# Kernel tuning notes

Measured on AMD Instinct MI355X. Metric: run time of the kernel, lower is better.

## Reference

```python
import jax, jax.numpy as jnp
import numpy as np

DIM = 1024
H_HEADS = 16


def setup_inputs() -> dict:
    key = jax.random.key(0)
    ks = jax.random.split(key, 12)
    h, w = 48, 80
    hw = h * w
    n_frames, n_sel = 11, 384
    wscale = 1.0 / np.sqrt(DIM).astype(np.float32)
    return {
        "feats_cur": jax.random.normal(ks[0], (1, DIM, h, w), jnp.float32),
        "ps": jax.random.normal(ks[1], (1, DIM, h, w), jnp.float32),
        "feats_ref": jax.random.normal(ks[2], (n_frames, DIM, h, w), jnp.float32),
        "ext_mem": jax.random.normal(ks[3], (24000, DIM), jnp.float32),
        "glob_cache": jax.random.normal(ks[4], (4000, DIM), jnp.float32),
        "Wq": jax.random.normal(ks[5], (DIM, DIM), jnp.float32) * wscale,
        "Wk": jax.random.normal(ks[6], (DIM, DIM), jnp.float32) * wscale,
        "Wv": jax.random.normal(ks[7], (DIM, DIM), jnp.float32) * wscale,
        "Wo": jax.random.normal(ks[8], (DIM, DIM), jnp.float32) * wscale,
        "ref_sel_idx": jax.random.randint(ks[9], (n_frames, n_sel), 0, hw, jnp.int32),
        "mem_idx": jax.random.randint(ks[10], (2000,), 0, 24000, jnp.int32),
        "glob_idx": jax.random.randint(ks[11], (2000,), 0, 4000, jnp.int32),
    }


def reference(feats_cur, ps, feats_ref, ext_mem, glob_cache, Wq, Wk, Wv, Wo,
              ref_sel_idx, mem_idx, glob_idx):
    b, dim, h, w = feats_cur.shape
    hw = h * w
    # current-frame pixels with positional encoding -> queries [hw, dim]
    q_in = (feats_cur + ps)[0].reshape(dim, hw).T
    # reference frames + ps -> [F, hw, dim], sparse randperm-style subsample via precomputed indices
    ref = (feats_ref + ps).reshape(-1, dim, hw).transpose(0, 2, 1)
    sel = jnp.take_along_axis(ref, ref_sel_idx[:, :, None], axis=1).reshape(-1, dim)
    # concat with subsampled external memory and global cache pixels
    k_in = jnp.concatenate([sel, ext_mem[mem_idx], glob_cache[glob_idx]], axis=0)  # [Nk, dim]
    dh = dim // H_HEADS
    scale = 1.0 / np.sqrt(dh).astype(np.float32)
    q = (q_in @ Wq).reshape(hw, H_HEADS, dh)
    k = (k_in @ Wk).reshape(-1, H_HEADS, dh)
    v = (k_in @ Wv).reshape(-1, H_HEADS, dh)
    logits = jnp.einsum('qhd,khd->hqk', q, k) * scale  # [H, hw, Nk]
    attn = jax.nn.softmax(logits, axis=-1)
    ctx = jnp.einsum('hqk,khd->qhd', attn, v).reshape(hw, dim)
    out = q_in + ctx @ Wo  # residual, like MEGA relation module
    # back to [1, dim, h, w] as in update_lm_pixel_with_transpose
    return out.T.reshape(1, dim, h, w)
```

## Files before the change

kernel.cpp:

```cpp
#include <hip/hip_runtime.h>

using u16 = unsigned short;
using bf16x8 = __attribute__((ext_vector_type(8))) short;
using f32x4  = __attribute__((ext_vector_type(4))) float;

#define DIM   1024
#define HW    3840
#define NSEL  4224
#define NK    8224
#define NKPAD 8320
#define NH    16
#define KVB   64
#define THR   50.0f

typedef __attribute__((address_space(1))) const unsigned GU;
typedef __attribute__((address_space(3))) unsigned LU;

__device__ __forceinline__ u16 f2bf(float x) {
    unsigned u = __float_as_uint(x);
    return (u16)((u + 0x7FFFu + ((u >> 16) & 1u)) >> 16);
}

__device__ __forceinline__ float exp2fast(float x) {
    return __builtin_amdgcn_exp2f(x);
}

__global__ void prep_kernel(const float* __restrict__ Wq, const float* __restrict__ Wk,
                            const float* __restrict__ Wv, const float* __restrict__ Wo,
                            const float* __restrict__ fc, const float* __restrict__ ps,
                            const float* __restrict__ fr, const float* __restrict__ em,
                            const float* __restrict__ gc, const int* __restrict__ sel,
                            const int* __restrict__ midx, const int* __restrict__ gidx,
                            u16* __restrict__ WT, u16* __restrict__ qin, u16* __restrict__ kin) {
    const int b = blockIdx.x;
    const int tid = threadIdx.x;
    if (b < 4096) {
        const int zz = b >> 10, yy = (b >> 5) & 31, xx = b & 31;
        const float* src = zz == 0 ? Wq : zz == 1 ? Wk : zz == 2 ? Wv : Wo;
        u16* dst = WT + (size_t)zz * DIM * DIM;
        __shared__ float t[32][33];
        const int n0 = xx * 32, k0 = yy * 32;
        const int tx = tid & 31, ty = tid >> 5;
#pragma unroll
        for (int j = 0; j < 4; ++j)
            t[ty + 8 * j][tx] = src[(size_t)(k0 + ty + 8 * j) * DIM + n0 + tx];
        __syncthreads();
#pragma unroll
        for (int j = 0; j < 4; ++j)
            dst[(size_t)(n0 + ty + 8 * j) * DIM + k0 + tx] = f2bf(t[tx][ty + 8 * j]);
    } else if (b < 7936) {
        const int bb = b - 4096;
        const int xx = bb % 120, yy = bb / 120;
        __shared__ float t[32][33];
        const int p0 = xx * 32, d0 = yy * 32;
        const int tx = tid & 31, ty = tid >> 5;
#pragma unroll
        for (int j = 0; j < 4; ++j) {
            int d = d0 + ty + 8 * j;
            t[ty + 8 * j][tx] = fc[(size_t)d * HW + p0 + tx] + ps[(size_t)d * HW + p0 + tx];
        }
        __syncthreads();
#pragma unroll
        for (int j = 0; j < 4; ++j)
            qin[(size_t)(p0 + ty + 8 * j) * DIM + d0 + tx] = f2bf(t[tx][ty + 8 * j]);
    } else {
        const int row = b - 7936;
        u16* dst = kin + (size_t)row * DIM;
        const int t = tid;
        if (row < NSEL) {
            const int f = row / 384;
            const int idx = sel[row];
            const float* base = fr + (size_t)f * DIM * HW + idx;
#pragma unroll
            for (int j = 0; j < 4; ++j) {
                int d = t + 256 * j;
                dst[d] = f2bf(base[(size_t)d * HW] + ps[(size_t)d * HW + idx]);
            }
        } else if (row < NSEL + 2000) {
            const float* src = em + (size_t)midx[row - NSEL] * DIM;
#pragma unroll
            for (int j = 0; j < 4; ++j) { int d = t + 256 * j; dst[d] = f2bf(src[d]); }
        } else if (row < NK) {
            const float* src = gc + (size_t)gidx[row - (NSEL + 2000)] * DIM;
#pragma unroll
            for (int j = 0; j < 4; ++j) { int d = t + 256 * j; dst[d] = f2bf(src[d]); }
        } else {
#pragma unroll
            for (int j = 0; j < 4; ++j) dst[t + 256 * j] = 0;
        }
    }
}

__device__ __forceinline__ void gemm_bt_body(const u16* __restrict__ A,
                                             const u16* __restrict__ B,
                                             void* __restrict__ Cout,
                                             const float* __restrict__ r1,
                                             const float* __restrict__ r2,
                                             int ldc, int mode, float scale,
                                             int bx, int by) {
    __shared__ __align__(16) u16 As[2][128 * 64];
    __shared__ __align__(16) u16 Bs[2][128 * 64];
    const int tid = threadIdx.x;
    const int l = tid & 63;
    const int wv = tid >> 6;
    const int wr = (wv >> 1) * 64, wc = (wv & 1) * 64;
    const int g = l >> 4, lo = l & 15;
    const size_t bm = (size_t)by * 128, bn = (size_t)bx * 128;
    const f32x4 fzero = {0.f, 0.f, 0.f, 0.f};

    f32x4 acc[4][4];
#pragma unroll
    for (int i = 0; i < 4; ++i)
#pragma unroll
        for (int j = 0; j < 4; ++j) acc[i][j] = fzero;

#define GSTAGE(BUF, KT)                                                                         \
    {                                                                                           \
        const int k0_ = (KT) * 64;                                                              \
        _Pragma("unroll") for (int q = 0; q < 4; ++q) {                                         \
            const int idx = q * 256 + tid;                                                      \
            const int row = idx >> 3, c8 = idx & 7;                                             \
            const int scol = (c8 ^ (row & 7)) * 8;                                              \
            const int dbase = q * 2048 + wv * 512;                                              \
            __builtin_amdgcn_global_load_lds((GU*)(A + (bm + row) * DIM + k0_ + scol),          \
                                             (LU*)&As[BUF][dbase], 16, 0, 0);                   \
            __builtin_amdgcn_global_load_lds((GU*)(B + (bn + row) * DIM + k0_ + scol),          \
                                             (LU*)&Bs[BUF][dbase], 16, 0, 0);                   \
        }                                                                                       \
    }

#define GCOMPUTE(BUF)                                                                           \
    {                                                                                           \
        _Pragma("unroll") for (int ks = 0; ks < 2; ++ks) {                                      \
            bf16x8 af[4], bfv[4];                                                               \
            _Pragma("unroll") for (int mi = 0; mi < 4; ++mi) {                                  \
                const int row = wr + mi * 16 + lo;                                              \
                const int sw = (ks * 4 + g) ^ (row & 7);                                        \
                af[mi] = *(const bf16x8*)(&As[BUF][row * 64 + sw * 8]);                         \
            }                                                                                   \
            _Pragma("unroll") for (int ni = 0; ni < 4; ++ni) {                                  \
                const int row = wc + ni * 16 + lo;                                              \
                const int sw = (ks * 4 + g) ^ (row & 7);                                        \
                bfv[ni] = *(const bf16x8*)(&Bs[BUF][row * 64 + sw * 8]);                        \
            }                                                                                   \
            _Pragma("unroll") for (int mi = 0; mi < 4; ++mi)                                    \
                _Pragma("unroll") for (int ni = 0; ni < 4; ++ni)                                \
                    acc[mi][ni] = __builtin_amdgcn_mfma_f32_16x16x32_bf16(af[mi], bfv[ni], acc[mi][ni], 0, 0, 0); \
        }                                                                                       \
    }

    GSTAGE(0, 0)
    asm volatile("s_waitcnt vmcnt(0)" ::: "memory");
    __syncthreads();

#pragma unroll 1
    for (int kt = 0; kt < 16; kt += 2) {
        GSTAGE(1, kt + 1)
        GCOMPUTE(0)
        asm volatile("s_waitcnt vmcnt(0)" ::: "memory");
        __syncthreads();
        if (kt + 2 < 16) GSTAGE(0, kt + 2)
        GCOMPUTE(1)
        asm volatile("s_waitcnt vmcnt(0)" ::: "memory");
        __syncthreads();
    }
#undef GCOMPUTE
#undef GSTAGE

    if (mode == 0) {
        u16* C = (u16*)Cout;
#pragma unroll
        for (int mi = 0; mi < 4; ++mi)
#pragma unroll
            for (int ni = 0; ni < 4; ++ni)
#pragma unroll
                for (int r = 0; r < 4; ++r) {
                    size_t m = bm + wr + mi * 16 + g * 4 + r;
                    size_t n = bn + wc + ni * 16 + lo;
                    C[m * (size_t)ldc + n] = f2bf(acc[mi][ni][r] * scale);
                }
    } else if (mode == 2) {
        u16* C = (u16*)Cout;
#pragma unroll
        for (int mi = 0; mi < 4; ++mi)
#pragma unroll
            for (int ni = 0; ni < 4; ++ni)
#pragma unroll
                for (int r = 0; r < 4; ++r) {
                    size_t m = bm + wr + mi * 16 + g * 4 + r;
                    size_t n = bn + wc + ni * 16 + lo;
                    size_t o = (n >> 6) * ((size_t)NKPAD * 64) + m * 64 + (n & 63);
                    C[o] = f2bf(acc[mi][ni][r] * scale);
                }
    } else {
        float* C = (float*)Cout;
#pragma unroll
        for (int mi = 0; mi < 4; ++mi)
#pragma unroll
            for (int ni = 0; ni < 4; ++ni)
#pragma unroll
                for (int r = 0; r < 4; ++r) {
                    size_t m = bm + wr + mi * 16 + g * 4 + r;
                    size_t n = bn + wc + ni * 16 + lo;
                    size_t o = m * (size_t)ldc + n;
                    C[o] = acc[mi][ni][r] + r1[o] + r2[o];
                }
    }
}

__global__ __launch_bounds__(256, 2) void proj_kernel(const u16* __restrict__ qin,
                                                      const u16* __restrict__ kin,
                                                      const u16* __restrict__ WT,
                                                      u16* __restrict__ Qp,
                                                      u16* __restrict__ Kp,
                                                      u16* __restrict__ Vt) {
    const int b = blockIdx.x;
    if (b < 240) {
        gemm_bt_body(qin, WT, Qp, nullptr, nullptr, 1024, 0, 0.18033688f, b % 8, b / 8);
    } else if (b < 760) {
        const int bb = b - 240;
        gemm_bt_body(kin, WT + 1048576, Kp, nullptr, nullptr, 1024, 2, 1.0f, bb % 8, bb / 8);
    } else {
        const int bb = b - 760;
        gemm_bt_body(WT + 2097152, kin, Vt, nullptr, nullptr, NKPAD, 0, 1.0f, bb % 65, bb / 65);
    }
}

__global__ __launch_bounds__(256, 2) void outproj_kernel(const u16* __restrict__ WTo,
                                                         const u16* __restrict__ ctx,
                                                         float* __restrict__ out,
                                                         const float* __restrict__ fc,
                                                         const float* __restrict__ ps) {
    gemm_bt_body(WTo, ctx, out, fc, ps, HW, 1, 1.0f, blockIdx.x, blockIdx.y);
}

__global__ __launch_bounds__(256, 3) void attn_kernel(const u16* __restrict__ Q,
                                                      const u16* __restrict__ Kh,
                                                      const u16* __restrict__ Vt,
                                                      u16* __restrict__ ctx) {
    __shared__ __align__(16) u16 Kl[2][4096];
    __shared__ __align__(16) u16 Vl[2][4096];
    __shared__ float invl_s[4][32];
    const int h = blockIdx.x;
    const int tid = threadIdx.x;
    const int l = tid & 63, wv = tid >> 6;
    const int g = l >> 4, lo = l & 15;
    const int hoff = h * 64;
    const int qw = blockIdx.y * 128 + wv * 32;
    const f32x4 fzero = {0.f, 0.f, 0.f, 0.f};
    const int sig = (lo >> 2) * 8 + (lo & 3);

    const u16* Ksrc = Kh + (size_t)h * NKPAD * 64;
    const u16* Vsrc = Vt + (size_t)hoff * NKPAD;

    bf16x8 qa[2][2];
#pragma unroll
    for (int mi = 0; mi < 2; ++mi)
#pragma unroll
        for (int ks = 0; ks < 2; ++ks)
            qa[mi][ks] = *(const bf16x8*)(Q + (size_t)(qw + mi * 16 + lo) * DIM + hoff + ks * 32 + g * 8);

    f32x4 acc[2][4];
#pragma unroll
    for (int mi = 0; mi < 2; ++mi)
#pragma unroll
        for (int ni = 0; ni < 4; ++ni) acc[mi][ni] = fzero;
    float mrow[2] = {-1e30f, -1e30f};
    float lsum[2] = {0.f, 0.f};
    float pmax[2] = {-1e30f, -1e30f};

#define STAGE(BUF, IT)                                                                          \
    {                                                                                           \
        const int kks = (IT) * KVB;                                                             \
        _Pragma("unroll") for (int j = 0; j < 2; ++j) {                                         \
            const int inst = wv * 2 + j;                                                        \
            const int r_ = inst * 8 + (l >> 3);                                                 \
            const int c_ = l & 7;                                                               \
            const int hk_ = ((l >> 3) & 3) | ((inst & 1) << 2);                                 \
            const u16* gK = Ksrc + (size_t)(kks + r_) * 64 + ((c_ ^ hk_) * 8);                  \
            __builtin_amdgcn_global_load_lds((GU*)gK, (LU*)&Kl[BUF][inst * 512], 16, 0, 0);     \
            const u16* gV = Vsrc + (size_t)r_ * NKPAD + kks + ((c_ ^ (r_ & 7)) * 8);            \
            __builtin_amdgcn_global_load_lds((GU*)gV, (LU*)&Vl[BUF][inst * 512], 16, 0, 0);     \
        }                                                                                       \
    }

#define COMPUTE(BUF, NT, NS)                                                                    \
    {                                                                                           \
        f32x4 S[2][4];                                                                          \
        _Pragma("unroll") for (int kp = 0; kp < (NT) / 2; ++kp) {                               \
            bf16x8 kf[2][2];                                                                    \
            _Pragma("unroll") for (int k2 = 0; k2 < 2; ++k2)                                    \
                _Pragma("unroll") for (int ks = 0; ks < 2; ++ks) {                              \
                    const int kt = kp * 2 + k2;                                                 \
                    const int row = (kt >> 1) * 32 + (kt & 1) * 4 + sig;                        \
                    const int hk_ = (row & 3) | (((row >> 3) & 1) << 2);                        \
                    const int ck = (ks * 4 + g) ^ hk_;                                          \
                    kf[k2][ks] = *(const bf16x8*)(&Kl[BUF][row * 64 + ck * 8]);                 \
                }                                                                               \
            _Pragma("unroll") for (int mi = 0; mi < 2; ++mi)                                    \
                _Pragma("unroll") for (int k2 = 0; k2 < 2; ++k2) {                              \
                    f32x4 s_ = __builtin_amdgcn_mfma_f32_16x16x32_bf16(kf[k2][0], qa[mi][0], fzero, 0, 0, 0); \
                    S[mi][kp * 2 + k2] = __builtin_amdgcn_mfma_f32_16x16x32_bf16(kf[k2][1], qa[mi][1], s_, 0, 0, 0); \
                }                                                                               \
        }                                                                                       \
        _Pragma("unroll") for (int mi = 0; mi < 2; ++mi)                                        \
            _Pragma("unroll") for (int kt = 0; kt < (NT); ++kt) {                               \
                f32x4 sv = S[mi][kt];                                                           \
                pmax[mi] = fmaxf(pmax[mi], fmaxf(fmaxf(sv[0], sv[1]), fmaxf(sv[2], sv[3])));    \
            }                                                                                   \
        if (__any(fmaxf(pmax[0] - mrow[0], pmax[1] - mrow[1]) > THR)) {                         \
            _Pragma("unroll") for (int mi = 0; mi < 2; ++mi) {                                  \
                float v = pmax[mi];                                                             \
                v = fmaxf(v, __shfl_xor(v, 16));                                                \
                v = fmaxf(v, __shfl_xor(v, 32));                                                \
                float mn = fmaxf(mrow[mi], v);                                                  \
                float fct = exp2fast(mrow[mi] - mn);                                            \
                mrow[mi] = mn;                                                                  \
                lsum[mi] *= fct;                                                                \
                _Pragma("unroll") for (int r = 0; r < 4; ++r) {                                 \
                    float fr_ = __shfl(fct, g * 4 + r);                                         \
                    _Pragma("unroll") for (int ni = 0; ni < 4; ++ni) acc[mi][ni][r] *= fr_;     \
                }                                                                               \
            }                                                                                   \
        }                                                                                       \
        _Pragma("unroll") for (int s = 0; s < (NS); ++s) {                                      \
            bf16x8 vb[4];                                                                       \
            _Pragma("unroll") for (int ni = 0; ni < 4; ++ni) {                                  \
                const int row = ni * 16 + lo;                                                   \
                const int ck = (s * 4 + g) ^ (row & 7);                                         \
                vb[ni] = *(const bf16x8*)(&Vl[BUF][row * 64 + ck * 8]);                         \
            }                                                                                   \
            _Pragma("unroll") for (int mi = 0; mi < 2; ++mi) {                                  \
                float p0 = exp2fast(S[mi][2 * s][0] - mrow[mi]);                                \
                float p1 = exp2fast(S[mi][2 * s][1] - mrow[mi]);                                \
                float p2 = exp2fast(S[mi][2 * s][2] - mrow[mi]);                                \
                float p3 = exp2fast(S[mi][2 * s][3] - mrow[mi]);                                \
                float p4 = exp2fast(S[mi][2 * s + 1][0] - mrow[mi]);                            \
                float p5 = exp2fast(S[mi][2 * s + 1][1] - mrow[mi]);                            \
                float p6 = exp2fast(S[mi][2 * s + 1][2] - mrow[mi]);                            \
                float p7 = exp2fast(S[mi][2 * s + 1][3] - mrow[mi]);                            \
                lsum[mi] += ((p0 + p1) + (p2 + p3)) + ((p4 + p5) + (p6 + p7));                  \
                union { unsigned u[4]; bf16x8 v; } pu;                                          \
                asm("v_cvt_pk_bf16_f32 %0, %1, %2" : "=v"(pu.u[0]) : "v"(p0), "v"(p1));         \
                asm("v_cvt_pk_bf16_f32 %0, %1, %2" : "=v"(pu.u[1]) : "v"(p2), "v"(p3));         \
                asm("v_cvt_pk_bf16_f32 %0, %1, %2" : "=v"(pu.u[2]) : "v"(p4), "v"(p5));         \
                asm("v_cvt_pk_bf16_f32 %0, %1, %2" : "=v"(pu.u[3]) : "v"(p6), "v"(p7));         \
                _Pragma("unroll") for (int ni = 0; ni < 4; ++ni)                                \
                    acc[mi][ni] = __builtin_amdgcn_mfma_f32_16x16x32_bf16(pu.v, vb[ni], acc[mi][ni], 0, 0, 0); \
            }                                                                                   \
        }                                                                                       \
    }

    STAGE(0, 0)
    asm volatile("s_waitcnt vmcnt(0)" ::: "memory");
    __syncthreads();

#pragma unroll 1
    for (int it = 0; it < 128; it += 2) {
        STAGE(1, it + 1)
        COMPUTE(0, 4, 2)
        asm volatile("s_waitcnt vmcnt(0)" ::: "memory");
        __syncthreads();
        STAGE(0, it + 2)
        COMPUTE(1, 4, 2)
        asm volatile("s_waitcnt vmcnt(0)" ::: "memory");
        __syncthreads();
    }
    COMPUTE(0, 2, 1)
#undef COMPUTE
#undef STAGE

#pragma unroll
    for (int mi = 0; mi < 2; ++mi) {
        float t = lsum[mi];
        t += __shfl_xor(t, 16);
        t += __shfl_xor(t, 32);
        lsum[mi] = t;
    }
    if (l < 16) {
        invl_s[wv][lo] = 1.0f / lsum[0];
        invl_s[wv][16 + lo] = 1.0f / lsum[1];
    }
#pragma unroll
    for (int mi = 0; mi < 2; ++mi)
#pragma unroll
        for (int ni = 0; ni < 4; ++ni)
#pragma unroll
            for (int r = 0; r < 4; ++r) {
                float val = acc[mi][ni][r] * invl_s[wv][mi * 16 + g * 4 + r];
                ctx[(size_t)(qw + mi * 16 + g * 4 + r) * DIM + hoff + ni * 16 + lo] = f2bf(val);
            }
}

extern "C" void kernel_launch(void* const* d_in, const int* in_sizes, int n_in,
                              void* d_out, int out_size, void* d_ws, size_t ws_size,
                              hipStream_t stream) {
    const float* fc  = (const float*)d_in[0];
    const float* ps  = (const float*)d_in[1];
    const float* fr  = (const float*)d_in[2];
    const float* em  = (const float*)d_in[3];
    const float* gc  = (const float*)d_in[4];
    const float* Wq  = (const float*)d_in[5];
    const float* Wk  = (const float*)d_in[6];
    const float* Wv  = (const float*)d_in[7];
    const float* Wo  = (const float*)d_in[8];
    const int* sel   = (const int*)d_in[9];
    const int* midx  = (const int*)d_in[10];
    const int* gidx  = (const int*)d_in[11];

    char* w = (char*)d_ws;
    u16* WT  = (u16*)(w);
    u16* qin = (u16*)(w + 8388608ull);
    u16* kin = (u16*)(w + 16252928ull);
    u16* Qp  = (u16*)(w + 33292288ull);
    u16* Kp  = (u16*)(w + 41156608ull);
    u16* Vt  = (u16*)(w + 58195968ull);
    u16* ctx = (u16*)(w + 75235328ull);
    float* out = (float*)d_out;

    prep_kernel<<<dim3(16256), dim3(256), 0, stream>>>(Wq, Wk, Wv, Wo, fc, ps, fr, em, gc,
                                                       sel, midx, gidx, WT, qin, kin);
    proj_kernel<<<dim3(1280), dim3(256), 0, stream>>>(qin, kin, WT, Qp, Kp, Vt);

    attn_kernel<<<dim3(NH, 30), dim3(256), 0, stream>>>(Qp, Kp, Vt, ctx);

    outproj_kernel<<<dim3(30, 8), dim3(256), 0, stream>>>(WT + 3145728, ctx, out, fc, ps);
}
```

Measured before the change: 403.2 us.

## Split attention KV range across wave pairs and merge partial softmax states

The attention kernel now gives each block 64 query rows instead of 128 and splits the key/value sequence between two wave pairs. Each pair streams its own half in 32-key tiles and keeps its own running max and sum. The two partial results are then merged through shared memory using a log-sum-exp rescale. The grid doubles to 960 blocks and the occupancy hint rises to 4 blocks per CU, to improve latency hiding and CU fill. In exchange, the kernel has smaller MFMA tiles per barrier, more synchronisation, and an extra reduction epilogue.

```diff
diff --git a/kernel.cpp b/kernel.cpp
--- a/kernel.cpp
+++ b/kernel.cpp
@@ -10,7 +10,6 @@
 #define NK    8224
 #define NKPAD 8320
 #define NH    16
-#define KVB   64
 #define THR   50.0f
 
 typedef __attribute__((address_space(1))) const unsigned GU;
@@ -234,21 +233,25 @@
     gemm_bt_body(WTo, ctx, out, fc, ps, HW, 1, 1.0f, blockIdx.x, blockIdx.y);
 }
 
-__global__ __launch_bounds__(256, 3) void attn_kernel(const u16* __restrict__ Q,
+__global__ __launch_bounds__(256, 4) void attn_kernel(const u16* __restrict__ Q,
                                                       const u16* __restrict__ Kh,
                                                       const u16* __restrict__ Vt,
                                                       u16* __restrict__ ctx) {
-    __shared__ __align__(16) u16 Kl[2][4096];
-    __shared__ __align__(16) u16 Vl[2][4096];
-    __shared__ float invl_s[4][32];
+    __shared__ __align__(16) u16 Kst[2][2][2048];
+    __shared__ __align__(16) u16 Vst[2][2][2048];
+    __shared__ float mlb[2][2][32][2];
+    __shared__ float mbuf2[2][32][20];
     const int h = blockIdx.x;
     const int tid = threadIdx.x;
     const int l = tid & 63, wv = tid >> 6;
+    const int qh = wv & 1, kh = wv >> 1;
     const int g = l >> 4, lo = l & 15;
     const int hoff = h * 64;
-    const int qw = blockIdx.y * 128 + wv * 32;
+    const int qw = blockIdx.y * 64 + qh * 32;
     const f32x4 fzero = {0.f, 0.f, 0.f, 0.f};
     const int sig = (lo >> 2) * 8 + (lo & 3);
+    const int W0 = kh * 128;
+    const int nw = 128 + kh;
 
     const u16* Ksrc = Kh + (size_t)h * NKPAD * 64;
     const u16* Vsrc = Vt + (size_t)hoff * NKPAD;
@@ -269,45 +272,46 @@
     float lsum[2] = {0.f, 0.f};
     float pmax[2] = {-1e30f, -1e30f};
 
-#define STAGE(BUF, IT)                                                                          \
+#define STAGE32(BUF, IT)                                                                        \
     {                                                                                           \
-        const int kks = (IT) * KVB;                                                             \
-        _Pragma("unroll") for (int j = 0; j < 2; ++j) {                                         \
-            const int inst = wv * 2 + j;                                                        \
-            const int r_ = inst * 8 + (l >> 3);                                                 \
-            const int c_ = l & 7;                                                               \
-            const int hk_ = ((l >> 3) & 3) | ((inst & 1) << 2);                                 \
-            const u16* gK = Ksrc + (size_t)(kks + r_) * 64 + ((c_ ^ hk_) * 8);                  \
-            __builtin_amdgcn_global_load_lds((GU*)gK, (LU*)&Kl[BUF][inst * 512], 16, 0, 0);     \
-            const u16* gV = Vsrc + (size_t)r_ * NKPAD + kks + ((c_ ^ (r_ & 7)) * 8);            \
-            __builtin_amdgcn_global_load_lds((GU*)gV, (LU*)&Vl[BUF][inst * 512], 16, 0, 0);     \
-        }                                                                                       \
-    }
-
-#define COMPUTE(BUF, NT, NS)                                                                    \
+        const int kk_ = (W0 + (IT)) * 32;                                                       \
+        _Pragma("unroll") for (int jj = 0; jj < 2; ++jj) {                                      \
+            const int j = qh * 2 + jj;                                                          \
+            const int rk = j * 8 + (l >> 3);                                                    \
+            const int hkk = (rk & 3) | (((rk >> 3) & 1) << 2);                                  \
+            const u16* gK = Ksrc + (size_t)(kk_ + rk) * 64 + (((l & 7) ^ hkk) * 8);             \
+            __builtin_amdgcn_global_load_lds((GU*)gK, (LU*)&Kst[kh][BUF][j * 512], 16, 0, 0);   \
+            const int xu = (l & 7) ^ (l >> 3);                                                  \
+            const int dv = 2 * rk + (xu >> 2);                                                  \
+            const u16* gV = Vsrc + (size_t)dv * NKPAD + kk_ + ((xu & 3) * 8);                   \
+            __builtin_amdgcn_global_load_lds((GU*)gV, (LU*)&Vst[kh][BUF][j * 512], 16, 0, 0);   \
+        }                                                                                       \
+    }
+
+#define COMPUTE32(BUF)                                                                          \
     {                                                                                           \
-        f32x4 S[2][4];                                                                          \
-        _Pragma("unroll") for (int kp = 0; kp < (NT) / 2; ++kp) {                               \
-            bf16x8 kf[2][2];                                                                    \
-            _Pragma("unroll") for (int k2 = 0; k2 < 2; ++k2)                                    \
-                _Pragma("unroll") for (int ks = 0; ks < 2; ++ks) {                              \
-                    const int kt = kp * 2 + k2;                                                 \
-                    const int row = (kt >> 1) * 32 + (kt & 1) * 4 + sig;                        \
-                    const int hk_ = (row & 3) | (((row >> 3) & 1) << 2);                        \
-                    const int ck = (ks * 4 + g) ^ hk_;                                          \
-                    kf[k2][ks] = *(const bf16x8*)(&Kl[BUF][row * 64 + ck * 8]);                 \
-                }                                                                               \
-            _Pragma("unroll") for (int mi = 0; mi < 2; ++mi)                                    \
-                _Pragma("unroll") for (int k2 = 0; k2 < 2; ++k2) {                              \
-                    f32x4 s_ = __builtin_amdgcn_mfma_f32_16x16x32_bf16(kf[k2][0], qa[mi][0], fzero, 0, 0, 0); \
-                    S[mi][kp * 2 + k2] = __builtin_amdgcn_mfma_f32_16x16x32_bf16(kf[k2][1], qa[mi][1], s_, 0, 0, 0); \
-                }                                                                               \
-        }                                                                                       \
-        _Pragma("unroll") for (int mi = 0; mi < 2; ++mi)                                        \
-            _Pragma("unroll") for (int kt = 0; kt < (NT); ++kt) {                               \
-                f32x4 sv = S[mi][kt];                                                           \
-                pmax[mi] = fmaxf(pmax[mi], fmaxf(fmaxf(sv[0], sv[1]), fmaxf(sv[2], sv[3])));    \
-            }                                                                                   \
+        bf16x8 kf0, kf1, kf2, kf3;                                                              \
+        {                                                                                       \
+            const int r0_ = sig, r1_ = sig + 4;                                                 \
+            const int h0_ = (r0_ & 3) | (((r0_ >> 3) & 1) << 2);                                \
+            const int h1_ = (r1_ & 3) | (((r1_ >> 3) & 1) << 2);                                \
+            kf0 = *(const bf16x8*)(&Kst[kh][BUF][r0_ * 64 + ((0 + g) ^ h0_) * 8]);              \
+            kf1 = *(const bf16x8*)(&Kst[kh][BUF][r0_ * 64 + ((4 + g) ^ h0_) * 8]);              \
+            kf2 = *(const bf16x8*)(&Kst[kh][BUF][r1_ * 64 + ((0 + g) ^ h1_) * 8]);              \
+            kf3 = *(const bf16x8*)(&Kst[kh][BUF][r1_ * 64 + ((4 + g) ^ h1_) * 8]);              \
+        }                                                                                       \
+        f32x4 S0[2], S1[2];                                                                     \
+        _Pragma("unroll") for (int mi = 0; mi < 2; ++mi) {                                      \
+            f32x4 s_ = __builtin_amdgcn_mfma_f32_16x16x32_bf16(kf0, qa[mi][0], fzero, 0, 0, 0); \
+            S0[mi] = __builtin_amdgcn_mfma_f32_16x16x32_bf16(kf1, qa[mi][1], s_, 0, 0, 0);      \
+            f32x4 t_ = __builtin_amdgcn_mfma_f32_16x16x32_bf16(kf2, qa[mi][0], fzero, 0, 0, 0); \
+            S1[mi] = __builtin_amdgcn_mfma_f32_16x16x32_bf16(kf3, qa[mi][1], t_, 0, 0, 0);      \
+        }                                                                                       \
+        _Pragma("unroll") for (int mi = 0; mi < 2; ++mi) {                                      \
+            float a_ = fmaxf(fmaxf(S0[mi][0], S0[mi][1]), fmaxf(S0[mi][2], S0[mi][3]));         \
+            float b_ = fmaxf(fmaxf(S1[mi][0], S1[mi][1]), fmaxf(S1[mi][2], S1[mi][3]));         \
+            pmax[mi] = fmaxf(pmax[mi], fmaxf(a_, b_));                                          \
+        }                                                                                       \
         if (__any(fmaxf(pmax[0] - mrow[0], pmax[1] - mrow[1]) > THR)) {                         \
             _Pragma("unroll") for (int mi = 0; mi < 2; ++mi) {                                  \
                 float v = pmax[mi];                                                             \
@@ -323,52 +327,52 @@
                 }                                                                               \
             }                                                                                   \
         }                                                                                       \
-        _Pragma("unroll") for (int s = 0; s < (NS); ++s) {                                      \
-            bf16x8 vb[4];                                                                       \
-            _Pragma("unroll") for (int ni = 0; ni < 4; ++ni) {                                  \
-                const int row = ni * 16 + lo;                                                   \
-                const int ck = (s * 4 + g) ^ (row & 7);                                         \
-                vb[ni] = *(const bf16x8*)(&Vl[BUF][row * 64 + ck * 8]);                         \
-            }                                                                                   \
-            _Pragma("unroll") for (int mi = 0; mi < 2; ++mi) {                                  \
-                float p0 = exp2fast(S[mi][2 * s][0] - mrow[mi]);                                \
-                float p1 = exp2fast(S[mi][2 * s][1] - mrow[mi]);                                \
-                float p2 = exp2fast(S[mi][2 * s][2] - mrow[mi]);                                \
-                float p3 = exp2fast(S[mi][2 * s][3] - mrow[mi]);                                \
-                float p4 = exp2fast(S[mi][2 * s + 1][0] - mrow[mi]);                            \
-                float p5 = exp2fast(S[mi][2 * s + 1][1] - mrow[mi]);                            \
-                float p6 = exp2fast(S[mi][2 * s + 1][2] - mrow[mi]);                            \
-                float p7 = exp2fast(S[mi][2 * s + 1][3] - mrow[mi]);                            \
-                lsum[mi] += ((p0 + p1) + (p2 + p3)) + ((p4 + p5) + (p6 + p7));                  \
-                union { unsigned u[4]; bf16x8 v; } pu;                                          \
-                asm("v_cvt_pk_bf16_f32 %0, %1, %2" : "=v"(pu.u[0]) : "v"(p0), "v"(p1));         \
-                asm("v_cvt_pk_bf16_f32 %0, %1, %2" : "=v"(pu.u[1]) : "v"(p2), "v"(p3));         \
-                asm("v_cvt_pk_bf16_f32 %0, %1, %2" : "=v"(pu.u[2]) : "v"(p4), "v"(p5));         \
-                asm("v_cvt_pk_bf16_f32 %0, %1, %2" : "=v"(pu.u[3]) : "v"(p6), "v"(p7));         \
-                _Pragma("unroll") for (int ni = 0; ni < 4; ++ni)                                \
-                    acc[mi][ni] = __builtin_amdgcn_mfma_f32_16x16x32_bf16(pu.v, vb[ni], acc[mi][ni], 0, 0, 0); \
-            }                                                                                   \
-        }                                                                                       \
-    }
-
-    STAGE(0, 0)
+        bf16x8 vb[4];                                                                           \
+        _Pragma("unroll") for (int ni = 0; ni < 4; ++ni) {                                      \
+            const int R_ = ni * 8 + (lo >> 1);                                                  \
+            const int ck_ = (((lo & 1) * 4 + g) ^ (lo >> 1)) * 8;                               \
+            vb[ni] = *(const bf16x8*)(&Vst[kh][BUF][R_ * 64 + ck_]);                            \
+        }                                                                                       \
+        _Pragma("unroll") for (int mi = 0; mi < 2; ++mi) {                                      \
+            float p0 = exp2fast(S0[mi][0] - mrow[mi]);                                          \
+            float p1 = exp2fast(S0[mi][1] - mrow[mi]);                                          \
+            float p2 = exp2fast(S0[mi][2] - mrow[mi]);                                          \
+            float p3 = exp2fast(S0[mi][3] - mrow[mi]);                                          \
+            float p4 = exp2fast(S1[mi][0] - mrow[mi]);                                          \
+            float p5 = exp2fast(S1[mi][1] - mrow[mi]);                                          \
+            float p6 = exp2fast(S1[mi][2] - mrow[mi]);                                          \
+            float p7 = exp2fast(S1[mi][3] - mrow[mi]);                                          \
+            lsum[mi] += ((p0 + p1) + (p2 + p3)) + ((p4 + p5) + (p6 + p7));                      \
+            union { unsigned u[4]; bf16x8 v; } pu;                                              \
+            asm("v_cvt_pk_bf16_f32 %0, %1, %2" : "=v"(pu.u[0]) : "v"(p0), "v"(p1));             \
+            asm("v_cvt_pk_bf16_f32 %0, %1, %2" : "=v"(pu.u[1]) : "v"(p2), "v"(p3));             \
+            asm("v_cvt_pk_bf16_f32 %0, %1, %2" : "=v"(pu.u[2]) : "v"(p4), "v"(p5));             \
+            asm("v_cvt_pk_bf16_f32 %0, %1, %2" : "=v"(pu.u[3]) : "v"(p6), "v"(p7));             \
+            _Pragma("unroll") for (int ni = 0; ni < 4; ++ni)                                    \
+                acc[mi][ni] = __builtin_amdgcn_mfma_f32_16x16x32_bf16(pu.v, vb[ni], acc[mi][ni], 0, 0, 0); \
+        }                                                                                       \
+    }
+
+    STAGE32(0, 0)
     asm volatile("s_waitcnt vmcnt(0)" ::: "memory");
     __syncthreads();
 
 #pragma unroll 1
-    for (int it = 0; it < 128; it += 2) {
-        STAGE(1, it + 1)
-        COMPUTE(0, 4, 2)
+    for (int it = 0; it + 1 < nw; it += 2) {
+        STAGE32(1, it + 1)
+        COMPUTE32(0)
         asm volatile("s_waitcnt vmcnt(0)" ::: "memory");
         __syncthreads();
-        STAGE(0, it + 2)
-        COMPUTE(1, 4, 2)
+        STAGE32(0, it + 2)
+        COMPUTE32(1)
         asm volatile("s_waitcnt vmcnt(0)" ::: "memory");
         __syncthreads();
     }
-    COMPUTE(0, 2, 1)
-#undef COMPUTE
-#undef STAGE
+    if (kh == 1) {
+        COMPUTE32(0)
+    }
+#undef COMPUTE32
+#undef STAGE32
 
 #pragma unroll
     for (int mi = 0; mi < 2; ++mi) {
@@ -378,18 +382,48 @@
         lsum[mi] = t;
     }
     if (l < 16) {
-        invl_s[wv][lo] = 1.0f / lsum[0];
-        invl_s[wv][16 + lo] = 1.0f / lsum[1];
-    }
+        mlb[kh][qh][lo][0] = mrow[0];
+        mlb[kh][qh][lo][1] = lsum[0];
+        mlb[kh][qh][16 + lo][0] = mrow[1];
+        mlb[kh][qh][16 + lo][1] = lsum[1];
+    }
+    __syncthreads();
+
+    float esf[2][4], inl[2][4];
 #pragma unroll
     for (int mi = 0; mi < 2; ++mi)
 #pragma unroll
-        for (int ni = 0; ni < 4; ++ni)
-#pragma unroll
-            for (int r = 0; r < 4; ++r) {
-                float val = acc[mi][ni][r] * invl_s[wv][mi * 16 + g * 4 + r];
-                ctx[(size_t)(qw + mi * 16 + g * 4 + r) * DIM + hoff + ni * 16 + lo] = f2bf(val);
-            }
+        for (int r = 0; r < 4; ++r) {
+            const int row = mi * 16 + g * 4 + r;
+            float m0 = mlb[0][qh][row][0], l0 = mlb[0][qh][row][1];
+            float m1 = mlb[1][qh][row][0], l1 = mlb[1][qh][row][1];
+            float M = fmaxf(m0, m1);
+            float e0 = exp2fast(m0 - M), e1 = exp2fast(m1 - M);
+            esf[mi][r] = kh ? e1 : e0;
+            inl[mi][r] = 1.0f / (l0 * e0 + l1 * e1);
+        }
+
+#pragma unroll
+    for (int ni = 0; ni < 4; ++ni) {
+        __syncthreads();
+        if (kh == 1) {
+#pragma unroll
+            for (int mi = 0; mi < 2; ++mi)
+#pragma unroll
+                for (int r = 0; r < 4; ++r)
+                    mbuf2[qh][mi * 16 + g * 4 + r][lo] = acc[mi][ni][r] * esf[mi][r];
+        }
+        __syncthreads();
+        if (kh == 0) {
+#pragma unroll
+            for (int mi = 0; mi < 2; ++mi)
+#pragma unroll
+                for (int r = 0; r < 4; ++r) {
+                    float val = (acc[mi][ni][r] * esf[mi][r] + mbuf2[qh][mi * 16 + g * 4 + r][lo]) * inl[mi][r];
+                    ctx[(size_t)(qw + mi * 16 + g * 4 + r) * DIM + hoff + ni * 16 + lo] = f2bf(val);
+                }
+        }
+    }
 }
 
 extern "C" void kernel_launch(void* const* d_in, const int* in_sizes, int n_in,
@@ -422,7 +456,7 @@
                                                        sel, midx, gidx, WT, qin, kin);
     proj_kernel<<<dim3(1280), dim3(256), 0, stream>>>(qin, kin, WT, Qp, Kp, Vt);
 
-    attn_kernel<<<dim3(NH, 30), dim3(256), 0, stream>>>(Qp, Kp, Vt, ctx);
+    attn_kernel<<<dim3(NH, 60), dim3(256), 0, stream>>>(Qp, Kp, Vt, ctx);
 
     outproj_kernel<<<dim3(30, 8), dim3(256), 0, stream>>>(WT + 3145728, ctx, out, fc, ps);
 }
```

Measured after the change: 421.3 us. 4.5% more time.
